# Kernel optimization log

Measured on AMD Instinct MI355X. Metric: run time of the kernel, lower is better.

The kernel has to match this reference:

```python
import jax, jax.numpy as jnp
import numpy as np

NO = 16          # config['Max_Object']
NT = 8           # config['Max_Time']
FEAT = 512       # config['feat_dims']
VIS_IN = 2048
TGT = 24


def setup_inputs() -> dict:
    key = jax.random.key(0)
    ks = jax.random.split(key, 10)
    b = 16
    N = NT * 2 * NO  # 256
    s = lambda k, *sh: jax.random.normal(k, sh, dtype=jnp.float32) * 0.02
    return {
        "src": jax.random.normal(ks[0], (b, 1, 1, N, VIS_IN), dtype=jnp.float32),
        "tgt_rel": jax.random.randint(ks[1], (b * NT * NO * NO,), 0, TGT, dtype=jnp.int64),
        "w1": s(ks[2], VIS_IN, FEAT), "b1": jnp.zeros((FEAT,), jnp.float32),
        "w2": s(ks[3], FEAT, FEAT),   "b2": jnp.zeros((FEAT,), jnp.float32),
        "wf": s(ks[4], FEAT, FEAT),   "bf": jnp.zeros((FEAT,), jnp.float32),
        "wr": s(ks[5], 2 * FEAT, TGT), "br": jnp.zeros((TGT,), jnp.float32),
    }


def reference(src, tgt_rel, w1, b1, w2, b2, wf, bf, wr, br):
    b = src.shape[0]
    BT = b * NT
    # src[:, 0, 0, :, :] -> (b, N, D) -> (b*NT, 2*NO, D); take visual part [:2048]
    x = src[:, 0, 0, :, :].reshape(BT, 2 * NO, -1)[:, :, :VIS_IN]
    # fc_vis: MLP 2048 -> FEAT -> FEAT
    h = jnp.maximum(x @ w1 + b1, 0.0) @ w2 + b2          # (BT, 2NO, FEAT)
    node_feats = h @ wf + bf                             # fc_fusion
    # vectorized replacement of the NOxNO python double loop:
    # edge[:, i*NO + (j-NO), :] = cat(node[:, i], node[:, j])  for i<NO<=j
    subj = jnp.broadcast_to(node_feats[:, :NO, None, :], (BT, NO, NO, FEAT))
    obj = jnp.broadcast_to(node_feats[:, None, NO:, :], (BT, NO, NO, FEAT))
    edge_feats = jnp.concatenate([subj, obj], axis=-1).reshape(BT, NO * NO, 2 * FEAT)
    out = (edge_feats @ wr + br).reshape(-1, TGT)        # fc_rel
    tgt = tgt_rel.reshape(-1)
    w_cls = jnp.asarray([1.0] + [100.0] * (TGT - 1), dtype=out.dtype)
    logp = jax.nn.log_softmax(out, axis=-1)
    nll = -jnp.take_along_axis(logp, tgt[:, None], axis=1)[:, 0]
    ww = w_cls[tgt]
    loss = jnp.sum(ww * nll) / jnp.sum(ww)  # torch weighted cross_entropy (mean)
    return out, tgt, loss
```

## Files before the change

### kernel.cpp

```cpp
#include <hip/hip_runtime.h>
#include <cstddef>
#include <cstdint>

#define NOBJ   16
#define FEAT   512
#define VIS    2048
#define NTGT   24
#define MROWS  4096
#define EROWS  32768

typedef __attribute__((ext_vector_type(8))) short short8;
typedef __attribute__((ext_vector_type(4))) float f32x4;

__device__ __forceinline__ float bf2f(unsigned short u) {
    union { unsigned int i; float f; } v; v.i = ((unsigned int)u) << 16; return v.f;
}
__device__ __forceinline__ unsigned short f2bf(float f) {
    union { float f; unsigned int i; } v; v.f = f;
    const unsigned int x = v.i;
    return (unsigned short)((x + 0x7fffu + ((x >> 16) & 1u)) >> 16);
}
__device__ __forceinline__ short8 pack8(const float4 a, const float4 b) {
    short8 r;
    r[0] = (short)f2bf(a.x); r[1] = (short)f2bf(a.y);
    r[2] = (short)f2bf(a.z); r[3] = (short)f2bf(a.w);
    r[4] = (short)f2bf(b.x); r[5] = (short)f2bf(b.y);
    r[6] = (short)f2bf(b.z); r[7] = (short)f2bf(b.w);
    return r;
}

__global__ __launch_bounds__(256)
void prep1(const float* __restrict__ w1, unsigned short* __restrict__ w1t,
           const float* __restrict__ wf, const float* __restrict__ bfv,
           const float* __restrict__ wr, float* __restrict__ t1) {
    __shared__ float shbuf[FEAT * NTGT];
    const int b   = blockIdx.x;
    const int tid = threadIdx.x;
    if (b < 1024) {
        float (*tile)[33] = (float(*)[33])shbuf;
        const int k0 = (b & 63) * 32;
        const int n0 = (b >> 6) * 32;
        const int tx = tid & 31, ty = tid >> 5;
        #pragma unroll
        for (int r = 0; r < 32; r += 8)
            tile[ty + r][tx] = w1[(size_t)(k0 + ty + r) * FEAT + n0 + tx];
        __syncthreads();
        #pragma unroll
        for (int r = 0; r < 32; r += 8)
            w1t[(size_t)(n0 + ty + r) * VIS + k0 + tx] = f2bf(tile[tx][ty + r]);
    } else {
        const int bb = b - 1024;
        const int h  = bb & 1;
        const float* wrh = wr + (size_t)h * FEAT * NTGT;
        for (int idx = tid; idx < FEAT * NTGT; idx += 256)
            shbuf[idx] = wrh[idx];
        __syncthreads();
        const int c    = tid & 31;
        const int krow = (bb >> 1) * 8 + (tid >> 5);
        if (krow > 512) return;
        const float* rowp = (krow < 512) ? (wf + (size_t)krow * FEAT) : bfv;
        const int ce = (c < NTGT) ? c : NTGT - 1;
        float s = 0.f;
        #pragma unroll 8
        for (int j = 0; j < FEAT; ++j)
            s = fmaf(rowp[j], shbuf[j * NTGT + ce], s);
        if (c < NTGT) t1[((size_t)h * 513 + krow) * 32 + c] = s;
    }
}

__global__ __launch_bounds__(256)
void prep2(const float* __restrict__ w2, const float* __restrict__ b2,
           const float* __restrict__ t1, unsigned short* __restrict__ wABt,
           float* __restrict__ biasAB, float* __restrict__ P) {
    __shared__ float shbuf[FEAT * NTGT];
    const int b   = blockIdx.x;
    const int tid = threadIdx.x;
    if (b < 1024) {
        P[(size_t)b * 256 + tid] = 0.f;
        return;
    }
    const int bb = b - 1024;
    const int h  = bb & 1;
    for (int idx = tid; idx < FEAT * NTGT; idx += 256) {
        const int row = idx / NTGT, col = idx - row * NTGT;
        shbuf[idx] = t1[((size_t)h * 513 + row) * 32 + col];
    }
    __syncthreads();
    const int c = tid & 31;
    const int r = (bb >> 1) * 8 + (tid >> 5);
    if (r > 512) return;
    const float* rowp = (r < 512) ? (w2 + (size_t)r * FEAT) : b2;
    const int ce = (c < NTGT) ? c : NTGT - 1;
    float s = 0.f;
    #pragma unroll 8
    for (int k = 0; k < FEAT; ++k)
        s = fmaf(rowp[k], shbuf[k * NTGT + ce], s);
    if (c < NTGT) {
        const int q = h * NTGT + c;
        if (r < 512) wABt[(size_t)q * FEAT + r] = f2bf(s);
        else         biasAB[q] = s + t1[((size_t)h * 513 + 512) * 32 + c];
    }
}

__global__ __launch_bounds__(256)
void gemm1f(const float* __restrict__ src, const unsigned short* __restrict__ w1t,
            const float* __restrict__ b1, const unsigned short* __restrict__ wABt,
            float* __restrict__ P) {
    __shared__ __align__(16) unsigned short As[2][64 * 64];
    __shared__ __align__(16) unsigned short Bs[2][32 * 64];

    const int bid = blockIdx.x;
    const int xcd = bid & 7;
    const int k8  = bid >> 3;
    const int xb  = k8 & 15;
    const int yb  = (xcd << 3) | (k8 >> 4);
    const int m0 = yb * 64;
    const int n0 = xb * 32;

    const int tid  = threadIdx.x;
    const int lane = tid & 63;
    const int wid  = tid >> 6;
    const int wr = wid >> 1, wc = wid & 1;

    f32x4  acc[2] = {};
    float4 areg[2][2];
    short8 breg;

    #pragma unroll
    for (int q = 0; q < 2; ++q) {
        const int s = q * 256 + tid, row = s >> 3, c = s & 7, cd = c ^ (row & 7);
        const float* gp = src + (size_t)(m0 + row) * VIS + (cd << 3);
        areg[q][0] = *reinterpret_cast<const float4*>(gp);
        areg[q][1] = *reinterpret_cast<const float4*>(gp + 4);
    }
    {
        const int n = tid >> 3, c = tid & 7, cd = c ^ (n & 7);
        breg = *reinterpret_cast<const short8*>(w1t + (size_t)(n0 + n) * VIS + (cd << 3));
    }
    #pragma unroll
    for (int q = 0; q < 2; ++q) {
        const int s = q * 256 + tid, row = s >> 3, c = s & 7;
        *reinterpret_cast<short8*>(&As[0][(row << 6) + (c << 3)]) = pack8(areg[q][0], areg[q][1]);
    }
    {
        const int n = tid >> 3, c = tid & 7;
        *reinterpret_cast<short8*>(&Bs[0][(n << 6) + (c << 3)]) = breg;
    }
    __syncthreads();

    int cur = 0;
    for (int t = 0; t < VIS / 64; ++t) {
        const int kn = (t + 1) * 64;
        if (t + 1 < VIS / 64) {
            #pragma unroll
            for (int q = 0; q < 2; ++q) {
                const int s = q * 256 + tid, row = s >> 3, c = s & 7, cd = c ^ (row & 7);
                const float* gp = src + (size_t)(m0 + row) * VIS + kn + (cd << 3);
                areg[q][0] = *reinterpret_cast<const float4*>(gp);
                areg[q][1] = *reinterpret_cast<const float4*>(gp + 4);
            }
            const int n = tid >> 3, c = tid & 7, cd = c ^ (n & 7);
            breg = *reinterpret_cast<const short8*>(w1t + (size_t)(n0 + n) * VIS + kn + (cd << 3));
        }
        #pragma unroll
        for (int k2 = 0; k2 < 2; ++k2) {
            short8 af[2], bfr;
            #pragma unroll
            for (int fr = 0; fr < 2; ++fr) {
                const int row = wr * 32 + fr * 16 + (lane & 15);
                const int cw  = ((k2 << 2) + (lane >> 4)) ^ (row & 7);
                af[fr] = *reinterpret_cast<const short8*>(&As[cur][(row << 6) + (cw << 3)]);
            }
            {
                const int n  = wc * 16 + (lane & 15);
                const int cw = ((k2 << 2) + (lane >> 4)) ^ (n & 7);
                bfr = *reinterpret_cast<const short8*>(&Bs[cur][(n << 6) + (cw << 3)]);
            }
            #pragma unroll
            for (int fr = 0; fr < 2; ++fr)
                acc[fr] = __builtin_amdgcn_mfma_f32_16x16x32_bf16(af[fr], bfr, acc[fr], 0, 0, 0);
        }
        if (t + 1 < VIS / 64) {
            const int nxt = cur ^ 1;
            #pragma unroll
            for (int q = 0; q < 2; ++q) {
                const int s = q * 256 + tid, row = s >> 3, c = s & 7;
                *reinterpret_cast<short8*>(&As[nxt][(row << 6) + (c << 3)]) =
                    pack8(areg[q][0], areg[q][1]);
            }
            const int n = tid >> 3, c = tid & 7;
            *reinterpret_cast<short8*>(&Bs[nxt][(n << 6) + (c << 3)]) = breg;
        }
        __syncthreads();
        cur ^= 1;
    }

    short8 bq[3];
    #pragma unroll
    for (int t3 = 0; t3 < 3; ++t3)
        bq[t3] = *reinterpret_cast<const short8*>(
            wABt + (size_t)(t3 * 16 + (lane & 15)) * FEAT + n0 + ((lane >> 4) << 3));

    unsigned short* Ht = &As[0][0];
    {
        const int nl   = wc * 16 + (lane & 15);
        const float bias = b1[n0 + nl];
        #pragma unroll
        for (int fr = 0; fr < 2; ++fr) {
            const int ml = wr * 32 + fr * 16 + ((lane >> 4) << 2);
            #pragma unroll
            for (int r = 0; r < 4; ++r) {
                const float v = fmaxf(acc[fr][r] + bias, 0.f);
                Ht[(ml + r) * 40 + nl] = f2bf(v);
            }
        }
    }
    __syncthreads();

    short8 aep;
    {
        const int m = wid * 16 + (lane & 15);
        aep = *reinterpret_cast<const short8*>(&Ht[m * 40 + ((lane >> 4) << 3)]);
    }
    const f32x4 pz = {0.f, 0.f, 0.f, 0.f};
    #pragma unroll
    for (int t3 = 0; t3 < 3; ++t3) {
        f32x4 pp = __builtin_amdgcn_mfma_f32_16x16x32_bf16(aep, bq[t3], pz, 0, 0, 0);
        const int q  = t3 * 16 + (lane & 15);
        const int mb = m0 + wid * 16 + ((lane >> 4) << 2);
        #pragma unroll
        for (int r = 0; r < 4; ++r)
            atomicAdd(&P[(size_t)(mb + r) * 64 + q], pp[r]);
    }
}

__global__ __launch_bounds__(256)
void out_loss_kernel(const float* __restrict__ P, const float* __restrict__ br,
                     const float* __restrict__ biasAB, const int* __restrict__ tgt,
                     float* __restrict__ out, float* __restrict__ out_tgt,
                     float* __restrict__ partials) {
    __shared__ float sm[32][49];
    const int bt  = blockIdx.x;
    const int tid = threadIdx.x;
    for (int idx = tid; idx < 32 * 48; idx += 256) {
        const int row = idx / 48, col = idx - row * 48;
        sm[row][col] = P[(size_t)(bt * 32 + row) * 64 + col];
    }
    __syncthreads();

    const int r  = bt * 256 + tid;
    const int i  = tid >> 4, j = tid & 15;
    const int tg = tgt[r];

    float vals[NTGT];
    float mx = -1e30f, vtg = 0.f;
    #pragma unroll
    for (int t = 0; t < NTGT; ++t) {
        const float cv = br[t] + biasAB[t] + biasAB[24 + t];
        const float v  = sm[i][t] + sm[16 + j][24 + t] + cv;
        vals[t] = v;
        mx = fmaxf(mx, v);
        if (t == tg) vtg = v;
    }
    float se = 0.f;
    #pragma unroll
    for (int t = 0; t < NTGT; ++t) se += expf(vals[t] - mx);
    const float lse = mx + logf(se);

    float4* o4 = reinterpret_cast<float4*>(out + (size_t)r * NTGT);
    #pragma unroll
    for (int q = 0; q < 6; ++q)
        o4[q] = make_float4(vals[q * 4], vals[q * 4 + 1], vals[q * 4 + 2], vals[q * 4 + 3]);
    out_tgt[r] = (float)tg;

    const float wcl = (tg == 0) ? 1.f : 100.f;
    float p1 = wcl * (lse - vtg);
    float p2 = wcl;
    #pragma unroll
    for (int off = 32; off > 0; off >>= 1) {
        p1 += __shfl_down(p1, off);
        p2 += __shfl_down(p2, off);
    }
    __shared__ float s1[4], s2[4];
    const int lane = tid & 63, wv = tid >> 6;
    if (lane == 0) { s1[wv] = p1; s2[wv] = p2; }
    __syncthreads();
    if (tid == 0) {
        partials[bt]       = s1[0] + s1[1] + s1[2] + s1[3];
        partials[128 + bt] = s2[0] + s2[1] + s2[2] + s2[3];
    }
}

__global__ void final_loss(const float* __restrict__ partials, float* __restrict__ loss) {
    const int t = threadIdx.x;
    float a = partials[t] + partials[t + 64];
    float b = partials[128 + t] + partials[192 + t];
    #pragma unroll
    for (int off = 32; off > 0; off >>= 1) {
        a += __shfl_down(a, off);
        b += __shfl_down(b, off);
    }
    if (t == 0) loss[0] = a / b;
}

extern "C" void kernel_launch(void* const* d_in, const int* in_sizes, int n_in,
                              void* d_out, int out_size, void* d_ws, size_t ws_size,
                              hipStream_t stream) {
    const float* src = (const float*)d_in[0];
    const int*   tgt = (const int*)d_in[1];
    const float* w1  = (const float*)d_in[2];
    const float* b1  = (const float*)d_in[3];
    const float* w2  = (const float*)d_in[4];
    const float* b2  = (const float*)d_in[5];
    const float* wf  = (const float*)d_in[6];
    const float* bfv = (const float*)d_in[7];
    const float* wr  = (const float*)d_in[8];
    const float* br  = (const float*)d_in[9];

    float* ws = (float*)d_ws;
    unsigned short* w1t  = (unsigned short*)(ws);
    float*          t1   = ws + 524288;
    unsigned short* wABt = (unsigned short*)(ws + 557056);
    float*          biasAB = ws + 569344;
    float*          P    = ws + 569408;
    float*          parts = ws + 831552;

    float* out_logits = (float*)d_out;
    float* out_tgt    = out_logits + (size_t)EROWS * NTGT;
    float* out_lossp  = out_tgt + EROWS;

    prep1<<<1154, 256, 0, stream>>>(w1, w1t, wf, bfv, wr, t1);
    prep2<<<1154, 256, 0, stream>>>(w2, b2, t1, wABt, biasAB, P);
    gemm1f<<<1024, 256, 0, stream>>>(src, w1t, b1, wABt, P);
    out_loss_kernel<<<128, 256, 0, stream>>>(P, br, biasAB, tgt,
                                             out_logits, out_tgt, parts);
    final_loss<<<1, 64, 0, stream>>>(parts, out_lossp);
}
```

Measured before the change: 156.5 us.

## Pre-convert src to bf16 and stream GEMM tiles via global_load_lds

Adds extra blocks to prep1 that convert the fp32 src activations to bf16 once into workspace. The first GEMM then loads bf16 A and B tiles straight into LDS with global_load_lds, removing register staging and the per-tile fp32-to-bf16 pack. This cuts the bytes each GEMM block re-reads for A and frees VGPRs and VALU work in the main loop. The cost is an extra full read and write pass over src, plus a larger workspace.

```diff
diff --git a/kernel.cpp b/kernel.cpp
--- a/kernel.cpp
+++ b/kernel.cpp
@@ -12,27 +12,23 @@
 typedef __attribute__((ext_vector_type(8))) short short8;
 typedef __attribute__((ext_vector_type(4))) float f32x4;
 
-__device__ __forceinline__ float bf2f(unsigned short u) {
-    union { unsigned int i; float f; } v; v.i = ((unsigned int)u) << 16; return v.f;
-}
 __device__ __forceinline__ unsigned short f2bf(float f) {
     union { float f; unsigned int i; } v; v.f = f;
     const unsigned int x = v.i;
     return (unsigned short)((x + 0x7fffu + ((x >> 16) & 1u)) >> 16);
 }
-__device__ __forceinline__ short8 pack8(const float4 a, const float4 b) {
-    short8 r;
-    r[0] = (short)f2bf(a.x); r[1] = (short)f2bf(a.y);
-    r[2] = (short)f2bf(a.z); r[3] = (short)f2bf(a.w);
-    r[4] = (short)f2bf(b.x); r[5] = (short)f2bf(b.y);
-    r[6] = (short)f2bf(b.z); r[7] = (short)f2bf(b.w);
-    return r;
+
+__device__ __forceinline__ void gload16(const unsigned short* g, unsigned short* l) {
+    __builtin_amdgcn_global_load_lds(
+        (const __attribute__((address_space(1))) unsigned int*)(const void*)g,
+        (__attribute__((address_space(3))) unsigned int*)(void*)l, 16, 0, 0);
 }
 
 __global__ __launch_bounds__(256)
 void prep1(const float* __restrict__ w1, unsigned short* __restrict__ w1t,
            const float* __restrict__ wf, const float* __restrict__ bfv,
-           const float* __restrict__ wr, float* __restrict__ t1) {
+           const float* __restrict__ wr, float* __restrict__ t1,
+           const float* __restrict__ src, unsigned short* __restrict__ srcb) {
     __shared__ float shbuf[FEAT * NTGT];
     const int b   = blockIdx.x;
     const int tid = threadIdx.x;
@@ -48,7 +44,7 @@
         #pragma unroll
         for (int r = 0; r < 32; r += 8)
             w1t[(size_t)(n0 + ty + r) * VIS + k0 + tx] = f2bf(tile[tx][ty + r]);
-    } else {
+    } else if (b < 1154) {
         const int bb = b - 1024;
         const int h  = bb & 1;
         const float* wrh = wr + (size_t)h * FEAT * NTGT;
@@ -65,6 +61,20 @@
         for (int j = 0; j < FEAT; ++j)
             s = fmaf(rowp[j], shbuf[j * NTGT + ce], s);
         if (c < NTGT) t1[((size_t)h * 513 + krow) * 32 + c] = s;
+    } else {
+        const int bb = b - 1154;
+        #pragma unroll
+        for (int q = 0; q < 4; ++q) {
+            const size_t i = (size_t)bb * 8192 + q * 2048 + tid * 8;
+            const float4 a = *reinterpret_cast<const float4*>(src + i);
+            const float4 c = *reinterpret_cast<const float4*>(src + i + 4);
+            short8 o;
+            o[0] = (short)f2bf(a.x); o[1] = (short)f2bf(a.y);
+            o[2] = (short)f2bf(a.z); o[3] = (short)f2bf(a.w);
+            o[4] = (short)f2bf(c.x); o[5] = (short)f2bf(c.y);
+            o[6] = (short)f2bf(c.z); o[7] = (short)f2bf(c.w);
+            *reinterpret_cast<short8*>(srcb + i) = o;
+        }
     }
 }
 
@@ -103,7 +113,7 @@
 }
 
 __global__ __launch_bounds__(256)
-void gemm1f(const float* __restrict__ src, const unsigned short* __restrict__ w1t,
+void gemm1f(const unsigned short* __restrict__ srcb, const unsigned short* __restrict__ w1t,
             const float* __restrict__ b1, const unsigned short* __restrict__ wABt,
             float* __restrict__ P) {
     __shared__ __align__(16) unsigned short As[2][64 * 64];
@@ -122,45 +132,31 @@
     const int wid  = tid >> 6;
     const int wr = wid >> 1, wc = wid & 1;
 
-    f32x4  acc[2] = {};
-    float4 areg[2][2];
-    short8 breg;
-
-    #pragma unroll
-    for (int q = 0; q < 2; ++q) {
-        const int s = q * 256 + tid, row = s >> 3, c = s & 7, cd = c ^ (row & 7);
-        const float* gp = src + (size_t)(m0 + row) * VIS + (cd << 3);
-        areg[q][0] = *reinterpret_cast<const float4*>(gp);
-        areg[q][1] = *reinterpret_cast<const float4*>(gp + 4);
-    }
-    {
-        const int n = tid >> 3, c = tid & 7, cd = c ^ (n & 7);
-        breg = *reinterpret_cast<const short8*>(w1t + (size_t)(n0 + n) * VIS + (cd << 3));
-    }
-    #pragma unroll
-    for (int q = 0; q < 2; ++q) {
-        const int s = q * 256 + tid, row = s >> 3, c = s & 7;
-        *reinterpret_cast<short8*>(&As[0][(row << 6) + (c << 3)]) = pack8(areg[q][0], areg[q][1]);
-    }
-    {
-        const int n = tid >> 3, c = tid & 7;
-        *reinterpret_cast<short8*>(&Bs[0][(n << 6) + (c << 3)]) = breg;
-    }
+    const int aRow0 = tid >> 3, aCd0 = (tid & 7) ^ (aRow0 & 7);
+    const int s1i   = 256 + tid;
+    const int aRow1 = s1i >> 3, aCd1 = (s1i & 7) ^ (aRow1 & 7);
+    const int bN    = tid >> 3, bCd = (tid & 7) ^ (bN & 7);
+    const size_t aOff0 = (size_t)(m0 + aRow0) * VIS + (aCd0 << 3);
+    const size_t aOff1 = (size_t)(m0 + aRow1) * VIS + (aCd1 << 3);
+    const size_t bOff  = (size_t)(n0 + bN) * VIS + (bCd << 3);
+    const int ldsA0 = (wid * 64) << 3;
+    const int ldsA1 = (256 + wid * 64) << 3;
+    const int ldsB  = (wid * 64) << 3;
+
+    f32x4 acc[2] = {};
+
+    gload16(srcb + aOff0, &As[0][ldsA0]);
+    gload16(srcb + aOff1, &As[0][ldsA1]);
+    gload16(w1t + bOff,  &Bs[0][ldsB]);
     __syncthreads();
 
     int cur = 0;
     for (int t = 0; t < VIS / 64; ++t) {
-        const int kn = (t + 1) * 64;
         if (t + 1 < VIS / 64) {
-            #pragma unroll
-            for (int q = 0; q < 2; ++q) {
-                const int s = q * 256 + tid, row = s >> 3, c = s & 7, cd = c ^ (row & 7);
-                const float* gp = src + (size_t)(m0 + row) * VIS + kn + (cd << 3);
-                areg[q][0] = *reinterpret_cast<const float4*>(gp);
-                areg[q][1] = *reinterpret_cast<const float4*>(gp + 4);
-            }
-            const int n = tid >> 3, c = tid & 7, cd = c ^ (n & 7);
-            breg = *reinterpret_cast<const short8*>(w1t + (size_t)(n0 + n) * VIS + kn + (cd << 3));
+            const int kn = (t + 1) * 64;
+            gload16(srcb + aOff0 + kn, &As[cur ^ 1][ldsA0]);
+            gload16(srcb + aOff1 + kn, &As[cur ^ 1][ldsA1]);
+            gload16(w1t + bOff + kn,  &Bs[cur ^ 1][ldsB]);
         }
         #pragma unroll
         for (int k2 = 0; k2 < 2; ++k2) {
@@ -180,17 +176,6 @@
             for (int fr = 0; fr < 2; ++fr)
                 acc[fr] = __builtin_amdgcn_mfma_f32_16x16x32_bf16(af[fr], bfr, acc[fr], 0, 0, 0);
         }
-        if (t + 1 < VIS / 64) {
-            const int nxt = cur ^ 1;
-            #pragma unroll
-            for (int q = 0; q < 2; ++q) {
-                const int s = q * 256 + tid, row = s >> 3, c = s & 7;
-                *reinterpret_cast<short8*>(&As[nxt][(row << 6) + (c << 3)]) =
-                    pack8(areg[q][0], areg[q][1]);
-            }
-            const int n = tid >> 3, c = tid & 7;
-            *reinterpret_cast<short8*>(&Bs[nxt][(n << 6) + (c << 3)]) = breg;
-        }
         __syncthreads();
         cur ^= 1;
     }
@@ -318,20 +303,21 @@
     const float* br  = (const float*)d_in[9];
 
     float* ws = (float*)d_ws;
-    unsigned short* w1t  = (unsigned short*)(ws);
-    float*          t1   = ws + 524288;
-    unsigned short* wABt = (unsigned short*)(ws + 557056);
-    float*          biasAB = ws + 569344;
-    float*          P    = ws + 569408;
-    float*          parts = ws + 831552;
+    unsigned short* w1t   = (unsigned short*)(ws);
+    unsigned short* srcb  = (unsigned short*)(ws + 524288);
+    float*          t1    = ws + 4718592;
+    unsigned short* wABt  = (unsigned short*)(ws + 4751424);
+    float*          biasAB = ws + 4763712;
+    float*          P     = ws + 4763776;
+    float*          parts = ws + 5025920;
 
     float* out_logits = (float*)d_out;
     float* out_tgt    = out_logits + (size_t)EROWS * NTGT;
     float* out_lossp  = out_tgt + EROWS;
 
-    prep1<<<1154, 256, 0, stream>>>(w1, w1t, wf, bfv, wr, t1);
+    prep1<<<2178, 256, 0, stream>>>(w1, w1t, wf, bfv, wr, t1, src, srcb);
     prep2<<<1154, 256, 0, stream>>>(w2, b2, t1, wABt, biasAB, P);
-    gemm1f<<<1024, 256, 0, stream>>>(src, w1t, b1, wABt, P);
+    gemm1f<<<1024, 256, 0, stream>>>(srcb, w1t, b1, wABt, P);
     out_loss_kernel<<<128, 256, 0, stream>>>(P, br, biasAB, tgt,
                                              out_logits, out_tgt, parts);
     final_loss<<<1, 64, 0, stream>>>(parts, out_lossp);
```

Result: slower. 160.8 us (+2.8%).
